# Kernel tuning notes

Measured on AMD Instinct MI355X. Metric: run time of the kernel, lower is better.

## Reference

```python
import jax, jax.numpy as jnp
import numpy as np

B, C, H, W = 32, 256, 56, 56
G, K, RED = 2, 7, 4
BN_EPS = 1e-5


def _conv2d(x, w, pad, groups=1, bias=None):
    # x: (N, Cin, H, W), w: (Cout, Cin/groups, kh, kw)
    y = jax.lax.conv_general_dilated(
        x, w, window_strides=(1, 1), padding=[(pad, pad), (pad, pad)],
        dimension_numbers=("NCHW", "OIHW", "NCHW"), feature_group_count=groups)
    if bias is not None:
        y = y + bias[None, :, None, None]
    return y


def setup_inputs() -> dict:
    key = jax.random.key(0)
    ks = jax.random.split(key, 5)
    return {
        "x": jax.random.normal(ks[0], (B, C, H, W), jnp.float32),
        "w_dyn": jax.random.normal(ks[1], (G, C, K, K), jnp.float32) * 0.02,
        "proj1_w": jax.random.normal(ks[2], (C // RED, C, 3, 3), jnp.float32) * 0.02,
        "bn_gamma": jnp.ones((C // RED,), jnp.float32),
        "bn_beta": jnp.zeros((C // RED,), jnp.float32),
        "proj2_w": jax.random.normal(ks[3], (C * G, C // RED, 3, 3), jnp.float32) * 0.02,
        "proj2_b": jnp.zeros((C * G,), jnp.float32),
    }


def reference(x, w_dyn, proj1_w, bn_gamma, bn_beta, proj2_w, proj2_b):
    b, c, h, w = x.shape
    # AdaptiveAvgPool2d((K, K)); H, W divisible by K -> exact mean over (H//K, W//K) windows
    pooled = x.reshape(b, c, K, h // K, K, w // K).mean(axis=(3, 5))  # (B, C, K, K)
    # proj: Conv3x3 (no bias, BN follows) -> BN (inference: mean=0, var=1) -> GELU -> Conv3x3
    hmid = _conv2d(pooled, proj1_w, pad=1)
    hmid = hmid * (bn_gamma / jnp.sqrt(1.0 + BN_EPS))[None, :, None, None] + bn_beta[None, :, None, None]
    hmid = jax.nn.gelu(hmid, approximate=False)
    scale = _conv2d(hmid, proj2_w, pad=1, bias=proj2_b)  # (B, G*C, K, K)
    scale = jax.nn.softmax(scale.reshape(b, G, c, K, K), axis=1)
    # per-sample dynamic depthwise kernel: softmax-weighted mix of G kernel banks
    dyn_w = jnp.einsum("bgckl,gckl->bckl", scale, w_dyn)  # (B, C, K, K)
    # depthwise conv with per-sample weights: groups = B*C
    y = _conv2d(x.reshape(1, b * c, h, w), dyn_w.reshape(b * c, 1, K, K),
                pad=K // 2, groups=b * c)
    return y.reshape(b, c, h, w)
```

## Files before the change

kernel.cpp:

```cpp
#include <hip/hip_runtime.h>
#include <math.h>

#define BB 32
#define CC 256
#define HH 56
#define WW 56
#define KP 49
#define CMID 64
#define HW 3136

#define RSTR 64
#define PROWS 62
#define PSZ (PROWS * RSTR)

__global__ __launch_bounds__(256) void transpose_w_kernel(const float* __restrict__ w1,
                                                          const float* __restrict__ w2,
                                                          float* __restrict__ w1t,
                                                          float* __restrict__ w2t) {
    int tid = blockIdx.x * 256 + threadIdx.x;
    if (tid < 147456) {
        int co = tid & 63, ct = tid >> 6;
        w1t[tid] = w1[co * 2304 + ct];
    }
    if (tid < 294912) {
        int co = tid & 511, ct = tid >> 9;
        w2t[tid] = w2[co * 576 + ct];
    }
}

__global__ __launch_bounds__(256) void pool_kernel(const float* __restrict__ x,
                                                   float* __restrict__ pooled) {
    int wv = threadIdx.x >> 6, lane = threadIdx.x & 63;
    int g = blockIdx.x * 4 + wv;
    if (lane < KP) {
        int ko = lane / 7, kw = lane - ko * 7;
        const float* base = x + (size_t)g * HW + (ko * 8) * WW + kw * 8;
        float s = 0.f;
        #pragma unroll
        for (int r = 0; r < 8; ++r) {
            float4 a = *(const float4*)(base + r * WW);
            float4 b4 = *(const float4*)(base + r * WW + 4);
            s += a.x + a.y + a.z + a.w + b4.x + b4.y + b4.z + b4.w;
        }
        pooled[(size_t)g * KP + lane] = s * (1.f / 64.f);
    }
}

__global__ __launch_bounds__(512) void conv1_kernel(const float* __restrict__ pooled,
                                                    const float* __restrict__ w1t,
                                                    const float* __restrict__ gamma,
                                                    const float* __restrict__ beta,
                                                    float* __restrict__ hmid) {
    int y = blockIdx.x, b = blockIdx.y;
    int wv = threadIdx.x >> 6, co = threadIdx.x & 63;
    __shared__ float red[8][7][64];
    float acc[7] = {0.f, 0.f, 0.f, 0.f, 0.f, 0.f, 0.f};
    const float* pb = pooled + (size_t)b * CC * KP;
    for (int ci = 0; ci < 32; ++ci) {
        int cin = wv * 32 + ci;
        const float* prow_base = pb + cin * KP;
        const float* wbase = w1t + (size_t)(cin * 9) * 64 + co;
        #pragma unroll
        for (int ky = 0; ky < 3; ++ky) {
            int iy = y + ky - 1;
            if (0 <= iy && iy < 7) {
                float s[9];
                s[0] = 0.f; s[8] = 0.f;
                const float* pr = prow_base + iy * 7;
                #pragma unroll
                for (int j = 0; j < 7; ++j) s[j + 1] = pr[j];
                const float* wr = wbase + ky * 3 * 64;
                float w0 = wr[0], w1v = wr[64], w2v = wr[128];
                #pragma unroll
                for (int xx = 0; xx < 7; ++xx)
                    acc[xx] += s[xx] * w0 + s[xx + 1] * w1v + s[xx + 2] * w2v;
            }
        }
    }
    #pragma unroll
    for (int xx = 0; xx < 7; ++xx) red[wv][xx][co] = acc[xx];
    __syncthreads();
    if (threadIdx.x < 448) {
        int xx = threadIdx.x >> 6, c2 = threadIdx.x & 63;
        float tot = 0.f;
        #pragma unroll
        for (int w = 0; w < 8; ++w) tot += red[w][xx][c2];
        float bnscale = gamma[c2] * rsqrtf(1.f + 1e-5f);
        float h = tot * bnscale + beta[c2];
        float g = 0.5f * h * (1.f + erff(h * 0.70710678118654752440f));
        hmid[((size_t)b * CMID + c2) * KP + y * 7 + xx] = g;
    }
}

__global__ __launch_bounds__(512) void conv2_kernel(const float* __restrict__ hmid,
                                                    const float* __restrict__ w2t,
                                                    const float* __restrict__ b2,
                                                    const float* __restrict__ wdyn,
                                                    float* __restrict__ dynw) {
    int y = blockIdx.x, b = blockIdx.y;
    int g = threadIdx.x >> 8, co = threadIdx.x & 255;
    __shared__ float redA[2][7][256];
    __shared__ float redB[2][7][256];
    float a0[7] = {}, a1[7] = {};
    const float* hb = hmid + (size_t)b * CMID * KP;
    for (int ci = 0; ci < 32; ++ci) {
        int cin = g * 32 + ci;
        const float* hrow_base = hb + cin * KP;
        const float* wbase = w2t + (size_t)(cin * 9) * 512 + co;
        #pragma unroll
        for (int ky = 0; ky < 3; ++ky) {
            int iy = y + ky - 1;
            if (0 <= iy && iy < 7) {
                float s[9];
                s[0] = 0.f; s[8] = 0.f;
                const float* hr = hrow_base + iy * 7;
                #pragma unroll
                for (int j = 0; j < 7; ++j) s[j + 1] = hr[j];
                const float* wr = wbase + ky * 3 * 512;
                float wa0 = wr[0],    wb0 = wr[256];
                float wa1 = wr[512],  wb1 = wr[768];
                float wa2 = wr[1024], wb2 = wr[1280];
                #pragma unroll
                for (int xx = 0; xx < 7; ++xx) {
                    float v0 = s[xx], v1 = s[xx + 1], v2 = s[xx + 2];
                    a0[xx] += v0 * wa0 + v1 * wa1 + v2 * wa2;
                    a1[xx] += v0 * wb0 + v1 * wb1 + v2 * wb2;
                }
            }
        }
    }
    #pragma unroll
    for (int xx = 0; xx < 7; ++xx) { redA[g][xx][co] = a0[xx]; redB[g][xx][co] = a1[xx]; }
    __syncthreads();
    if (threadIdx.x < 256) {
        int c = threadIdx.x;
        float bias0 = b2[c], bias1 = b2[c + CC];
        const float* wd0 = wdyn + (size_t)c * KP + y * 7;
        const float* wd1 = wdyn + (size_t)(CC + c) * KP + y * 7;
        float* dw = dynw + ((size_t)(b * CC + c)) * KP + y * 7;
        #pragma unroll
        for (int xx = 0; xx < 7; ++xx) {
            float s0 = redA[0][xx][c] + redA[1][xx][c] + bias0;
            float s1 = redB[0][xx][c] + redB[1][xx][c] + bias1;
            float m = fmaxf(s0, s1);
            float e0 = expf(s0 - m), e1 = expf(s1 - m);
            dw[xx] = (e0 * wd0[xx] + e1 * wd1[xx]) / (e0 + e1);
        }
    }
}

__global__ __launch_bounds__(256) void dwconv_kernel(const float* __restrict__ x,
                                                     const float* __restrict__ dynw,
                                                     float* __restrict__ out) {
    __shared__ float xs[4 * PSZ];
    int tid = threadIdx.x;
    int g0 = blockIdx.x * 4;

    float4* xs4 = (float4*)xs;
    for (int e = tid; e < 4 * PSZ / 4; e += 256)
        xs4[e] = make_float4(0.f, 0.f, 0.f, 0.f);
    __syncthreads();

    for (int idx = tid; idx < 4 * 56 * 14; idx += 256) {
        int p   = idx / 784;
        int rem = idx - p * 784;
        int r   = rem / 14;
        int c4  = rem - r * 14;
        float4 v = *((const float4*)(x + ((size_t)(g0 + p)) * HW + r * WW) + c4);
        int pr    = r + 3;
        int shift = 4 * ((pr >> 3) & 7);
        int col   = (4 * c4 + 4 + shift) & 63;
        *(float4*)(xs + p * PSZ + pr * RSTR + col) = v;
    }
    __syncthreads();

    int wv = tid >> 6, lane = tid & 63;
    int gplane = __builtin_amdgcn_readfirstlane(g0 + wv);
    const float* wp = dynw + (size_t)gplane * KP;
    float w[49];
    #pragma unroll
    for (int i = 0; i < 49; ++i) w[i] = wp[i];

    if (lane < KP) {
        int ty = lane / 7, tx = lane - ty * 7;
        int r0 = 8 * ty, c0 = 8 * tx;
        const float* pbase = xs + wv * PSZ;
        float acc[8][8] = {};
        #pragma unroll
        for (int ir = 0; ir < 14; ++ir) {
            int pr = r0 + ir;
            int shift = 4 * ((pr >> 3) & 7);
            const float* rowp = pbase + pr * RSTR;
            float rb[16];
            #pragma unroll
            for (int k = 0; k < 4; ++k) {
                int col = (c0 + shift + 4 * k) & 63;
                float4 v = *(const float4*)(rowp + col);
                rb[4 * k + 0] = v.x; rb[4 * k + 1] = v.y;
                rb[4 * k + 2] = v.z; rb[4 * k + 3] = v.w;
            }
            #pragma unroll
            for (int ky = 0; ky < 7; ++ky) {
                int oy = ir - ky;
                if (0 <= oy && oy < 8) {
                    #pragma unroll
                    for (int kx = 0; kx < 7; ++kx) {
                        float ww = w[ky * 7 + kx];
                        #pragma unroll
                        for (int ox = 0; ox < 8; ++ox)
                            acc[oy][ox] += rb[ox + 1 + kx] * ww;
                    }
                }
            }
        }
        float* op = out + (size_t)(g0 + wv) * HW;
        #pragma unroll
        for (int oy = 0; oy < 8; ++oy) {
            float* orow = op + (r0 + oy) * WW + c0;
            *(float4*)(orow)     = make_float4(acc[oy][0], acc[oy][1], acc[oy][2], acc[oy][3]);
            *(float4*)(orow + 4) = make_float4(acc[oy][4], acc[oy][5], acc[oy][6], acc[oy][7]);
        }
    }
}

extern "C" void kernel_launch(void* const* d_in, const int* in_sizes, int n_in,
                              void* d_out, int out_size, void* d_ws, size_t ws_size,
                              hipStream_t stream) {
    const float* x     = (const float*)d_in[0];
    const float* wdyn  = (const float*)d_in[1];
    const float* w1    = (const float*)d_in[2];
    const float* gamma = (const float*)d_in[3];
    const float* beta  = (const float*)d_in[4];
    const float* w2    = (const float*)d_in[5];
    const float* b2    = (const float*)d_in[6];
    float* out = (float*)d_out;

    float* ws     = (float*)d_ws;
    float* pooled = ws;
    float* hmid   = ws + 401408;
    float* dynw   = ws + 501760;
    float* w1t    = ws + 903168;
    float* w2t    = ws + 1050624;

    transpose_w_kernel<<<dim3(1152),        256, 0, stream>>>(w1, w2, w1t, w2t);
    pool_kernel       <<<dim3(BB * CC / 4), 256, 0, stream>>>(x, pooled);
    conv1_kernel      <<<dim3(7, BB),       512, 0, stream>>>(pooled, w1t, gamma, beta, hmid);
    conv2_kernel      <<<dim3(7, BB),       512, 0, stream>>>(hmid, w2t, b2, wdyn, dynw);
    dwconv_kernel     <<<dim3(BB * CC / 4), 256, 0, stream>>>(x, dynw, out);
}
```

Before: 323.5 us.

## Fuse pooling with tiled weight transpose; one-plane-per-block depthwise conv

Pooling and both weight transposes are merged into a single launch, and the transposes now go through a 64x65 shared-memory tile so both reads and writes are coalesced. The depthwise conv now gives each 64-thread block one plane, with 56 threads each computing a 7x8 tile instead of 49 threads each doing 8x8. It also zeroes only the padding cells rather than clearing all of shared memory, and uses a per-row swizzle. The aim is less launch overhead, better lane usage, more resident blocks and less redundant shared-memory work, at the cost of smaller blocks and more row-overlap reads per output.

```diff
diff --git a/kernel.cpp b/kernel.cpp
--- a/kernel.cpp
+++ b/kernel.cpp
@@ -13,36 +13,51 @@
 #define PROWS 62
 #define PSZ (PROWS * RSTR)
 
-__global__ __launch_bounds__(256) void transpose_w_kernel(const float* __restrict__ w1,
-                                                          const float* __restrict__ w2,
-                                                          float* __restrict__ w1t,
-                                                          float* __restrict__ w2t) {
-    int tid = blockIdx.x * 256 + threadIdx.x;
-    if (tid < 147456) {
-        int co = tid & 63, ct = tid >> 6;
-        w1t[tid] = w1[co * 2304 + ct];
-    }
-    if (tid < 294912) {
-        int co = tid & 511, ct = tid >> 9;
-        w2t[tid] = w2[co * 576 + ct];
-    }
-}
-
-__global__ __launch_bounds__(256) void pool_kernel(const float* __restrict__ x,
-                                                   float* __restrict__ pooled) {
-    int wv = threadIdx.x >> 6, lane = threadIdx.x & 63;
-    int g = blockIdx.x * 4 + wv;
-    if (lane < KP) {
-        int ko = lane / 7, kw = lane - ko * 7;
-        const float* base = x + (size_t)g * HW + (ko * 8) * WW + kw * 8;
-        float s = 0.f;
-        #pragma unroll
-        for (int r = 0; r < 8; ++r) {
-            float4 a = *(const float4*)(base + r * WW);
-            float4 b4 = *(const float4*)(base + r * WW + 4);
-            s += a.x + a.y + a.z + a.w + b4.x + b4.y + b4.z + b4.w;
-        }
-        pooled[(size_t)g * KP + lane] = s * (1.f / 64.f);
+__global__ __launch_bounds__(256) void pre_kernel(const float* __restrict__ x,
+                                                  const float* __restrict__ w1,
+                                                  const float* __restrict__ w2,
+                                                  float* __restrict__ pooled,
+                                                  float* __restrict__ w1t,
+                                                  float* __restrict__ w2t) {
+    int bid = blockIdx.x;
+    if (bid < 2048) {
+        int wv = threadIdx.x >> 6, lane = threadIdx.x & 63;
+        int g = bid * 4 + wv;
+        if (lane < KP) {
+            int ko = lane / 7, kw = lane - ko * 7;
+            const float* base = x + (size_t)g * HW + (ko * 8) * WW + kw * 8;
+            float s = 0.f;
+            #pragma unroll
+            for (int r = 0; r < 8; ++r) {
+                float4 a = *(const float4*)(base + r * WW);
+                float4 b4 = *(const float4*)(base + r * WW + 4);
+                s += a.x + a.y + a.z + a.w + b4.x + b4.y + b4.z + b4.w;
+            }
+            pooled[(size_t)g * KP + lane] = s * (1.f / 64.f);
+        }
+        return;
+    }
+    __shared__ float t[64][65];
+    int r = threadIdx.x >> 6, c = threadIdx.x & 63;
+    if (bid < 2048 + 36) {
+        int ct0 = (bid - 2048) * 64;
+        #pragma unroll
+        for (int i = 0; i < 16; ++i)
+            t[r + 4 * i][c] = w1[(size_t)(r + 4 * i) * 2304 + ct0 + c];
+        __syncthreads();
+        #pragma unroll
+        for (int i = 0; i < 16; ++i)
+            w1t[(size_t)(ct0 + r + 4 * i) * 64 + c] = t[c][r + 4 * i];
+    } else {
+        int tt = bid - 2048 - 36;
+        int co0 = (tt / 9) * 64, ct0 = (tt % 9) * 64;
+        #pragma unroll
+        for (int i = 0; i < 16; ++i)
+            t[r + 4 * i][c] = w2[(size_t)(co0 + r + 4 * i) * 576 + ct0 + c];
+        __syncthreads();
+        #pragma unroll
+        for (int i = 0; i < 16; ++i)
+            w2t[(size_t)(ct0 + r + 4 * i) * 512 + co0 + c] = t[c][r + 4 * i];
     }
 }
 
@@ -149,48 +164,53 @@
     }
 }
 
-__global__ __launch_bounds__(256) void dwconv_kernel(const float* __restrict__ x,
-                                                     const float* __restrict__ dynw,
-                                                     float* __restrict__ out) {
-    __shared__ float xs[4 * PSZ];
+__global__ __launch_bounds__(64, 4) void dwconv_kernel(const float* __restrict__ x,
+                                                       const float* __restrict__ dynw,
+                                                       float* __restrict__ out) {
+    __shared__ __align__(16) float xs[PSZ];
     int tid = threadIdx.x;
-    int g0 = blockIdx.x * 4;
-
-    float4* xs4 = (float4*)xs;
-    for (int e = tid; e < 4 * PSZ / 4; e += 256)
-        xs4[e] = make_float4(0.f, 0.f, 0.f, 0.f);
-    __syncthreads();
-
-    for (int idx = tid; idx < 4 * 56 * 14; idx += 256) {
-        int p   = idx / 784;
-        int rem = idx - p * 784;
-        int r   = rem / 14;
-        int c4  = rem - r * 14;
-        float4 v = *((const float4*)(x + ((size_t)(g0 + p)) * HW + r * WW) + c4);
-        int pr    = r + 3;
-        int shift = 4 * ((pr >> 3) & 7);
-        int col   = (4 * c4 + 4 + shift) & 63;
-        *(float4*)(xs + p * PSZ + pr * RSTR + col) = v;
-    }
-    __syncthreads();
-
-    int wv = tid >> 6, lane = tid & 63;
-    int gplane = __builtin_amdgcn_readfirstlane(g0 + wv);
-    const float* wp = dynw + (size_t)gplane * KP;
+    int g = blockIdx.x;
+
+    const float* wp = dynw + (size_t)g * KP;
     float w[49];
     #pragma unroll
     for (int i = 0; i < 49; ++i) w[i] = wp[i];
 
-    if (lane < KP) {
-        int ty = lane / 7, tx = lane - ty * 7;
-        int r0 = 8 * ty, c0 = 8 * tx;
-        const float* pbase = xs + wv * PSZ;
-        float acc[8][8] = {};
-        #pragma unroll
-        for (int ir = 0; ir < 14; ++ir) {
+    for (int idx = tid; idx < 208; idx += 64) {
+        int pr, col;
+        if (idx < 96) {
+            int rowi = idx >> 4, c4 = idx & 15;
+            pr = rowi < 3 ? rowi : rowi + 56;
+            col = 4 * c4;
+        } else {
+            int i = idx - 96;
+            int rr = i >> 1;
+            pr = rr + 3;
+            int shift = 4 * (pr & 7);
+            col = (i & 1) ? ((shift + 60) & 63) : shift;
+        }
+        *(float4*)(xs + pr * RSTR + col) = make_float4(0.f, 0.f, 0.f, 0.f);
+    }
+
+    for (int idx = tid; idx < 784; idx += 64) {
+        int rr = idx / 14, c4 = idx - rr * 14;
+        float4 v = *((const float4*)(x + (size_t)g * HW + rr * WW) + c4);
+        int pr = rr + 3;
+        int shift = 4 * (pr & 7);
+        int col = (4 * c4 + 4 + shift) & 63;
+        *(float4*)(xs + pr * RSTR + col) = v;
+    }
+    __syncthreads();
+
+    if (tid < 56) {
+        int ty = tid / 7, tx = tid - ty * 7;
+        int r0 = 7 * ty, c0 = 8 * tx;
+        float acc[7][8] = {};
+        #pragma unroll
+        for (int ir = 0; ir < 13; ++ir) {
             int pr = r0 + ir;
-            int shift = 4 * ((pr >> 3) & 7);
-            const float* rowp = pbase + pr * RSTR;
+            int shift = 4 * (pr & 7);
+            const float* rowp = xs + pr * RSTR;
             float rb[16];
             #pragma unroll
             for (int k = 0; k < 4; ++k) {
@@ -202,7 +222,7 @@
             #pragma unroll
             for (int ky = 0; ky < 7; ++ky) {
                 int oy = ir - ky;
-                if (0 <= oy && oy < 8) {
+                if (0 <= oy && oy < 7) {
                     #pragma unroll
                     for (int kx = 0; kx < 7; ++kx) {
                         float ww = w[ky * 7 + kx];
@@ -213,9 +233,9 @@
                 }
             }
         }
-        float* op = out + (size_t)(g0 + wv) * HW;
-        #pragma unroll
-        for (int oy = 0; oy < 8; ++oy) {
+        float* op = out + (size_t)g * HW;
+        #pragma unroll
+        for (int oy = 0; oy < 7; ++oy) {
             float* orow = op + (r0 + oy) * WW + c0;
             *(float4*)(orow)     = make_float4(acc[oy][0], acc[oy][1], acc[oy][2], acc[oy][3]);
             *(float4*)(orow + 4) = make_float4(acc[oy][4], acc[oy][5], acc[oy][6], acc[oy][7]);
@@ -242,9 +262,8 @@
     float* w1t    = ws + 903168;
     float* w2t    = ws + 1050624;
 
-    transpose_w_kernel<<<dim3(1152),        256, 0, stream>>>(w1, w2, w1t, w2t);
-    pool_kernel       <<<dim3(BB * CC / 4), 256, 0, stream>>>(x, pooled);
-    conv1_kernel      <<<dim3(7, BB),       512, 0, stream>>>(pooled, w1t, gamma, beta, hmid);
-    conv2_kernel      <<<dim3(7, BB),       512, 0, stream>>>(hmid, w2t, b2, wdyn, dynw);
-    dwconv_kernel     <<<dim3(BB * CC / 4), 256, 0, stream>>>(x, dynw, out);
-}
+    pre_kernel   <<<dim3(2048 + 36 + 72), 256, 0, stream>>>(x, w1, w2, pooled, w1t, w2t);
+    conv1_kernel <<<dim3(7, BB),          512, 0, stream>>>(pooled, w1t, gamma, beta, hmid);
+    conv2_kernel <<<dim3(7, BB),          512, 0, stream>>>(hmid, w2t, b2, wdyn, dynw);
+    dwconv_kernel<<<dim3(BB * CC),         64, 0, stream>>>(x, dynw, out);
+}
```

New measurement: 321.0 us. About the same (-0.8%).
